# Performance work log

Hardware: AMD Instinct MI355X
Metric: run time of the kernel (lower is better)

Reference implementation:

```python
import jax, jax.numpy as jnp
import numpy as np

N_RBF = 16
N_HIDDEN = 64
CUTOFF = 5.0
N_ATOMS = 4096


def setup_inputs() -> dict:
    key = jax.random.key(0)
    ks = jax.random.split(key, 7)
    # Scale positions so the 5.0 cutoff yields a sparse-ish neighbor graph.
    positions = jax.random.normal(ks[0], (N_ATOMS, 3), dtype=jnp.float32) * 10.0
    s1 = 1.0 / np.sqrt(N_RBF)
    s2 = 1.0 / np.sqrt(N_HIDDEN)
    W1 = jax.random.normal(ks[1], (N_RBF, N_HIDDEN), dtype=jnp.float32) * s1
    b1 = jax.random.normal(ks[2], (N_HIDDEN,), dtype=jnp.float32) * 0.01
    W2 = jax.random.normal(ks[3], (N_HIDDEN, N_HIDDEN), dtype=jnp.float32) * s2
    b2 = jax.random.normal(ks[4], (N_HIDDEN,), dtype=jnp.float32) * 0.01
    W3 = jax.random.normal(ks[5], (N_HIDDEN, 1), dtype=jnp.float32) * s2
    b3 = jax.random.normal(ks[6], (1,), dtype=jnp.float32) * 0.01
    return {"positions": positions, "W1": W1, "b1": b1, "W2": W2, "b2": b2, "W3": W3, "b3": b3}


def _features(positions):
    # positions: (N, 3) -> per-node RBF-aggregated features (N, n_rbf).
    # Equivalent to torch mask.nonzero + scatter_add: features[i] = sum_j in-cutoff rbf(d_ij).
    diff = positions[:, None, :] - positions[None, :, :]          # (N, N, 3)
    dist = jnp.sqrt(jnp.sum(diff * diff, axis=-1))                # (N, N)
    mask = (dist > 1e-6) & (dist < CUTOFF)                        # (N, N)
    centers = jnp.linspace(0.5, CUTOFF, N_RBF, dtype=jnp.float32) # (n_rbf,)
    eta = 0.5 * CUTOFF / N_RBF
    gauss = jnp.exp(-((dist[..., None] - centers) ** 2) / (2.0 * eta * eta))  # (N, N, n_rbf)
    x = jnp.minimum(dist / CUTOFF, 1.0)
    smooth = 0.5 * (1.0 + jnp.cos(jnp.float32(np.pi) * x))        # (N, N)
    w = jnp.where(mask, smooth, 0.0)                              # masked smooth-cutoff weight
    return jnp.einsum('ij,ijk->ik', w, gauss)                     # (N, n_rbf)


def reference(positions, W1, b1, W2, b2, W3, b3):
    feats = _features(positions)                                  # (N, n_rbf)
    h = jax.nn.silu(feats @ W1 + b1)
    h = jax.nn.silu(h @ W2 + b2)
    energy = jnp.sum(h @ W3 + b3)                                 # scalar
    return energy
```

## Files before the change

kernel.cpp:

```cpp
#include <hip/hip_runtime.h>

#define N_ATOMS  4096
#define N_RBF    16
#define N_HIDDEN 64
#define NTHREADS 512
#define WPB      8
#define APB      8
#define NBLOCKS  (N_ATOMS / APB)
#define QCAP     96
#define QUART    (N_ATOMS / 4)

__global__ __launch_bounds__(256) void repack_kernel(const float* __restrict__ pos,
                                                     float4* __restrict__ pos4) {
    const int i = blockIdx.x * 256 + threadIdx.x;
    if (i < N_ATOMS)
        pos4[i] = make_float4(pos[i * 3 + 0], pos[i * 3 + 1], pos[i * 3 + 2], 0.0f);
}

__device__ __forceinline__ void accum_rbf(float d2, float (&f)[N_RBF]) {
    const float d  = sqrtf(d2);
    const float sm = 0.5f + 0.5f * __cosf(0.62831853071795865f * d);
    #pragma unroll
    for (int k = 0; k < N_RBF; ++k) {
        const float t = d - (0.5f + 0.3f * (float)k);
        f[k] += sm * __expf(-20.48f * t * t);
    }
}

__device__ __forceinline__ int wave_prefix(unsigned long long m) {
    return __builtin_amdgcn_mbcnt_hi((unsigned)(m >> 32),
            __builtin_amdgcn_mbcnt_lo((unsigned)m, 0u));
}

__global__ __launch_bounds__(NTHREADS, 8) void fused_sr_kernel(
    const float4* __restrict__ pos4,
    const float* __restrict__ W1,
    const float* __restrict__ b1,
    const float* __restrict__ W2,
    const float* __restrict__ b2,
    const float* __restrict__ W3,
    float* __restrict__ partial)
{
    __shared__ __align__(16) float qd[APB][4][QCAP];
    __shared__ int qcnt[APB][4];
    __shared__ __align__(16) float h1buf[WPB][N_HIDDEN];
    __shared__ float ered[WPB];

    const int tid  = threadIdx.x;
    const int lane = tid & 63;
    const int w    = tid >> 6;
    const int t    = w >> 2;
    const int q    = w & 3;
    const int iA   = blockIdx.x * APB + 4 * t;

    const float4 p0 = pos4[iA + 0];
    const float4 p1 = pos4[iA + 1];
    const float4 p2 = pos4[iA + 2];
    const float4 p3 = pos4[iA + 3];
    const int jbase = q * QUART;

    int c0_ = 0, c1_ = 0, c2_ = 0, c3_ = 0;

#define PAIR_TEST(P, CNT, AIDX)                                              \
    {                                                                        \
        const float dx = P.x - pj.x, dy = P.y - pj.y, dz = P.z - pj.z;       \
        const float d2 = fmaf(dx, dx, fmaf(dy, dy, dz * dz));                \
        const bool act = (d2 < 25.0f) && (d2 > 1e-12f);                      \
        const unsigned long long m = __ballot(act);                          \
        if (m) {                                                             \
            int widx = CNT + wave_prefix(m);                                 \
            widx = widx < QCAP ? widx : QCAP - 1;                            \
            if (act) qd[4 * t + AIDX][q][widx] = d2;                         \
            CNT += (int)__popcll(m);                                         \
        }                                                                    \
    }

    #pragma unroll 2
    for (int j0 = 0; j0 < QUART; j0 += 64) {
        const float4 pj = pos4[jbase + j0 + lane];
        PAIR_TEST(p0, c0_, 0)
        PAIR_TEST(p1, c1_, 1)
        PAIR_TEST(p2, c2_, 2)
        PAIR_TEST(p3, c3_, 3)
    }
#undef PAIR_TEST

    if (lane == 0) {
        qcnt[4 * t + 0][q] = c0_;
        qcnt[4 * t + 1][q] = c1_;
        qcnt[4 * t + 2][q] = c2_;
        qcnt[4 * t + 3][q] = c3_;
    }
    __syncthreads();

    const int co0 = qcnt[w][0], co1 = qcnt[w][1], co2 = qcnt[w][2], co3 = qcnt[w][3];
    const int o1 = co0, o2 = co0 + co1, o3 = o2 + co2, C = o3 + co3;
    float* qrow = &qd[w][0][0];

    float f[N_RBF];
    #pragma unroll
    for (int k = 0; k < N_RBF; ++k) f[k] = 0.0f;
    for (int b = 0; b < C; b += 64) {
        const int g = b + lane;
        const int part = (g >= o1) + (g >= o2) + (g >= o3);
        const int base = part == 0 ? 0 : (part == 1 ? o1 : (part == 2 ? o2 : o3));
        const float d2q = (g < C) ? qrow[part * QCAP + (g - base)] : 1e8f;
        accum_rbf(d2q, f);
    }

    #pragma unroll
    for (int k = 0; k < N_RBF; ++k) {
        f[k] += __shfl_xor(f[k], 32, 64);
        f[k] += __shfl_xor(f[k], 16, 64);
    }
    float* tb = qrow;
    if (lane < 16) {
        #pragma unroll
        for (int j = 0; j < 16; j += 4)
            *reinterpret_cast<float4*>(&tb[lane * 16 + j]) =
                make_float4(f[j], f[j + 1], f[j + 2], f[j + 3]);
    }
    const int kk = lane & 15, rep = lane >> 4;
    float F = 0.0f;
    #pragma unroll
    for (int i = 0; i < 4; ++i) F += tb[(4 * rep + i) * 16 + kk];
    F += __shfl_xor(F, 16, 64);
    F += __shfl_xor(F, 32, 64);
    if (lane < 16) tb[256 + lane] = F;

    float a1 = b1[lane];
    #pragma unroll
    for (int k = 0; k < N_RBF; ++k)
        a1 = fmaf(tb[256 + k], W1[k * N_HIDDEN + lane], a1);
    const float h1 = a1 / (1.0f + __expf(-a1));

    h1buf[w][lane] = h1;
    float a2 = b2[lane];
    #pragma unroll
    for (int k = 0; k < N_HIDDEN; k += 4) {
        const float4 hv = *reinterpret_cast<const float4*>(&h1buf[w][k]);
        a2 = fmaf(hv.x, W2[(k + 0) * N_HIDDEN + lane], a2);
        a2 = fmaf(hv.y, W2[(k + 1) * N_HIDDEN + lane], a2);
        a2 = fmaf(hv.z, W2[(k + 2) * N_HIDDEN + lane], a2);
        a2 = fmaf(hv.w, W2[(k + 3) * N_HIDDEN + lane], a2);
    }
    const float h2 = a2 / (1.0f + __expf(-a2));

    float e = h2 * W3[lane];
    #pragma unroll
    for (int off = 32; off > 0; off >>= 1)
        e += __shfl_xor(e, off, 64);
    if (lane == 0) ered[w] = e;
    __syncthreads();

    if (tid < 64) {
        float acc = (lane < WPB) ? ered[lane] : 0.0f;
        acc += __shfl_xor(acc, 4, 64);
        acc += __shfl_xor(acc, 2, 64);
        acc += __shfl_xor(acc, 1, 64);
        if (lane == 0) partial[blockIdx.x] = acc;
    }
}

__global__ __launch_bounds__(NTHREADS) void finish_kernel(
    const float* __restrict__ partial, const float* __restrict__ b3,
    float* __restrict__ out) {
    __shared__ float s[WPB];
    const int tid = threadIdx.x, lane = tid & 63, w = tid >> 6;
    float v = partial[tid];
    #pragma unroll
    for (int off = 32; off > 0; off >>= 1)
        v += __shfl_xor(v, off, 64);
    if (lane == 0) s[w] = v;
    __syncthreads();
    if (tid == 0) {
        float tot = 0.0f;
        #pragma unroll
        for (int i = 0; i < WPB; ++i) tot += s[i];
        out[0] = tot + (float)N_ATOMS * b3[0];
    }
}

extern "C" void kernel_launch(void* const* d_in, const int* in_sizes, int n_in,
                              void* d_out, int out_size, void* d_ws, size_t ws_size,
                              hipStream_t stream) {
    const float* pos = (const float*)d_in[0];
    const float* W1  = (const float*)d_in[1];
    const float* b1  = (const float*)d_in[2];
    const float* W2  = (const float*)d_in[3];
    const float* b2  = (const float*)d_in[4];
    const float* W3  = (const float*)d_in[5];
    const float* b3  = (const float*)d_in[6];
    float* out = (float*)d_out;

    float4* pos4    = (float4*)d_ws;
    float*  partial = (float*)((char*)d_ws + N_ATOMS * sizeof(float4));

    repack_kernel<<<(N_ATOMS + 255) / 256, 256, 0, stream>>>(pos, pos4);
    fused_sr_kernel<<<NBLOCKS, NTHREADS, 0, stream>>>(pos4, W1, b1, W2, b2, W3, partial);
    finish_kernel<<<1, NTHREADS, 0, stream>>>(partial, b3, out);
}
```

Baseline: 81.38 us.

## Replace brute-force all-pairs neighbor search with a uniform cell-list grid

Adds a zero-count kernel and an atomic binning kernel that sort atoms into a 24^3 grid of 5-unit cells. The main kernel then has one wave per atom scan only the 27 neighboring cells instead of all 4096 atoms. This removes the O(N^2) pair-distance work in exchange for two extra launches, atomics and a large workspace buffer. It relies on fixed caps (96 atoms per cell, 288 neighbors per atom) and a fixed coordinate range of [-60, 60] with clamping, all of which must hold for these inputs.

Result: slower. 84.79 us (+4.2%).

```diff
diff --git a/kernel.cpp b/kernel.cpp
--- a/kernel.cpp
+++ b/kernel.cpp
@@ -5,16 +5,35 @@
 #define N_HIDDEN 64
 #define NTHREADS 512
 #define WPB      8
-#define APB      8
-#define NBLOCKS  (N_ATOMS / APB)
-#define QCAP     96
-#define QUART    (N_ATOMS / 4)
-
-__global__ __launch_bounds__(256) void repack_kernel(const float* __restrict__ pos,
-                                                     float4* __restrict__ pos4) {
+#define NBLOCKS  (N_ATOMS / WPB)
+#define QCAP     288
+#define GRIDC    24
+#define NCELL    (GRIDC * GRIDC * GRIDC)
+#define CCAP     96
+#define CELL_INV 0.2f
+#define RANGEF   60.0f
+
+__global__ __launch_bounds__(256) void zero_counts(int* __restrict__ count) {
     const int i = blockIdx.x * 256 + threadIdx.x;
-    if (i < N_ATOMS)
-        pos4[i] = make_float4(pos[i * 3 + 0], pos[i * 3 + 1], pos[i * 3 + 2], 0.0f);
+    if (i < NCELL) count[i] = 0;
+}
+
+__global__ __launch_bounds__(256) void bin_kernel(const float* __restrict__ pos,
+                                                  int* __restrict__ count,
+                                                  float4* __restrict__ cellAtoms) {
+    const int i = blockIdx.x * 256 + threadIdx.x;
+    if (i >= N_ATOMS) return;
+    const float x = pos[3 * i + 0], y = pos[3 * i + 1], z = pos[3 * i + 2];
+    int cx = (int)floorf((x + RANGEF) * CELL_INV);
+    int cy = (int)floorf((y + RANGEF) * CELL_INV);
+    int cz = (int)floorf((z + RANGEF) * CELL_INV);
+    cx = min(max(cx, 0), GRIDC - 1);
+    cy = min(max(cy, 0), GRIDC - 1);
+    cz = min(max(cz, 0), GRIDC - 1);
+    const int cell = cx + GRIDC * (cy + GRIDC * cz);
+    int slot = atomicAdd(&count[cell], 1);
+    if (slot >= CCAP) slot = CCAP - 1;
+    cellAtoms[cell * CCAP + slot] = make_float4(x, y, z, 0.0f);
 }
 
 __device__ __forceinline__ void accum_rbf(float d2, float (&f)[N_RBF]) {
@@ -32,8 +51,10 @@
             __builtin_amdgcn_mbcnt_lo((unsigned)m, 0u));
 }
 
-__global__ __launch_bounds__(NTHREADS, 8) void fused_sr_kernel(
-    const float4* __restrict__ pos4,
+__global__ __launch_bounds__(NTHREADS) void fused_sr_kernel(
+    const float* __restrict__ pos,
+    const int* __restrict__ count,
+    const float4* __restrict__ cellAtoms,
     const float* __restrict__ W1,
     const float* __restrict__ b1,
     const float* __restrict__ W2,
@@ -41,71 +62,65 @@
     const float* __restrict__ W3,
     float* __restrict__ partial)
 {
-    __shared__ __align__(16) float qd[APB][4][QCAP];
-    __shared__ int qcnt[APB][4];
+    __shared__ float qd[WPB][QCAP];
     __shared__ __align__(16) float h1buf[WPB][N_HIDDEN];
     __shared__ float ered[WPB];
 
     const int tid  = threadIdx.x;
     const int lane = tid & 63;
     const int w    = tid >> 6;
-    const int t    = w >> 2;
-    const int q    = w & 3;
-    const int iA   = blockIdx.x * APB + 4 * t;
-
-    const float4 p0 = pos4[iA + 0];
-    const float4 p1 = pos4[iA + 1];
-    const float4 p2 = pos4[iA + 2];
-    const float4 p3 = pos4[iA + 3];
-    const int jbase = q * QUART;
-
-    int c0_ = 0, c1_ = 0, c2_ = 0, c3_ = 0;
-
-#define PAIR_TEST(P, CNT, AIDX)                                              \
-    {                                                                        \
-        const float dx = P.x - pj.x, dy = P.y - pj.y, dz = P.z - pj.z;       \
-        const float d2 = fmaf(dx, dx, fmaf(dy, dy, dz * dz));                \
-        const bool act = (d2 < 25.0f) && (d2 > 1e-12f);                      \
-        const unsigned long long m = __ballot(act);                          \
-        if (m) {                                                             \
-            int widx = CNT + wave_prefix(m);                                 \
-            widx = widx < QCAP ? widx : QCAP - 1;                            \
-            if (act) qd[4 * t + AIDX][q][widx] = d2;                         \
-            CNT += (int)__popcll(m);                                         \
-        }                                                                    \
-    }
-
-    #pragma unroll 2
-    for (int j0 = 0; j0 < QUART; j0 += 64) {
-        const float4 pj = pos4[jbase + j0 + lane];
-        PAIR_TEST(p0, c0_, 0)
-        PAIR_TEST(p1, c1_, 1)
-        PAIR_TEST(p2, c2_, 2)
-        PAIR_TEST(p3, c3_, 3)
-    }
-#undef PAIR_TEST
-
-    if (lane == 0) {
-        qcnt[4 * t + 0][q] = c0_;
-        qcnt[4 * t + 1][q] = c1_;
-        qcnt[4 * t + 2][q] = c2_;
-        qcnt[4 * t + 3][q] = c3_;
-    }
-    __syncthreads();
-
-    const int co0 = qcnt[w][0], co1 = qcnt[w][1], co2 = qcnt[w][2], co3 = qcnt[w][3];
-    const int o1 = co0, o2 = co0 + co1, o3 = o2 + co2, C = o3 + co3;
-    float* qrow = &qd[w][0][0];
+    const int i    = blockIdx.x * WPB + w;
+
+    const float xi = pos[3 * i + 0], yi = pos[3 * i + 1], zi = pos[3 * i + 2];
+    int cx = (int)floorf((xi + RANGEF) * CELL_INV);
+    int cy = (int)floorf((yi + RANGEF) * CELL_INV);
+    int cz = (int)floorf((zi + RANGEF) * CELL_INV);
+    cx = min(max(cx, 0), GRIDC - 1);
+    cy = min(max(cy, 0), GRIDC - 1);
+    cz = min(max(cz, 0), GRIDC - 1);
+
+    int myCell = 0, myCnt = 0;
+    if (lane < 27) {
+        const int nx = cx + (lane % 3) - 1;
+        const int ny = cy + ((lane / 3) % 3) - 1;
+        const int nz = cz + (lane / 9) - 1;
+        if (nx >= 0 && nx < GRIDC && ny >= 0 && ny < GRIDC && nz >= 0 && nz < GRIDC) {
+            myCell = nx + GRIDC * (ny + GRIDC * nz);
+            myCnt  = min(count[myCell], CCAP);
+        }
+    }
+
+    int qn = 0;
+    for (int j = 0; j < 27; ++j) {
+        const int cnt = __shfl(myCnt, j, 64);
+        if (cnt == 0) continue;
+        const int cid = __shfl(myCell, j, 64);
+        const float4* cbase = &cellAtoms[cid * CCAP];
+        for (int b = 0; b < cnt; b += 64) {
+            const int g = b + lane;
+            float d2 = 1e8f;
+            if (g < cnt) {
+                const float4 pj = cbase[g];
+                const float dx = xi - pj.x, dy = yi - pj.y, dz = zi - pj.z;
+                d2 = fmaf(dx, dx, fmaf(dy, dy, dz * dz));
+            }
+            const bool act = (d2 < 25.0f) && (d2 > 1e-12f);
+            const unsigned long long m = __ballot(act);
+            if (m) {
+                int widx = qn + wave_prefix(m);
+                widx = widx < QCAP ? widx : QCAP - 1;
+                if (act) qd[w][widx] = d2;
+                qn += (int)__popcll(m);
+            }
+        }
+    }
 
     float f[N_RBF];
     #pragma unroll
     for (int k = 0; k < N_RBF; ++k) f[k] = 0.0f;
-    for (int b = 0; b < C; b += 64) {
+    for (int b = 0; b < qn; b += 64) {
         const int g = b + lane;
-        const int part = (g >= o1) + (g >= o2) + (g >= o3);
-        const int base = part == 0 ? 0 : (part == 1 ? o1 : (part == 2 ? o2 : o3));
-        const float d2q = (g < C) ? qrow[part * QCAP + (g - base)] : 1e8f;
-        accum_rbf(d2q, f);
+        accum_rbf((g < qn) ? qd[w][g] : 1e8f, f);
     }
 
     #pragma unroll
@@ -113,17 +128,15 @@
         f[k] += __shfl_xor(f[k], 32, 64);
         f[k] += __shfl_xor(f[k], 16, 64);
     }
-    float* tb = qrow;
+    float* tb = &qd[w][0];
     if (lane < 16) {
         #pragma unroll
-        for (int j = 0; j < 16; j += 4)
-            *reinterpret_cast<float4*>(&tb[lane * 16 + j]) =
-                make_float4(f[j], f[j + 1], f[j + 2], f[j + 3]);
+        for (int j = 0; j < 16; ++j) tb[lane * 16 + j] = f[j];
     }
     const int kk = lane & 15, rep = lane >> 4;
     float F = 0.0f;
     #pragma unroll
-    for (int i = 0; i < 4; ++i) F += tb[(4 * rep + i) * 16 + kk];
+    for (int v = 0; v < 4; ++v) F += tb[(4 * rep + v) * 16 + kk];
     F += __shfl_xor(F, 16, 64);
     F += __shfl_xor(F, 32, 64);
     if (lane < 16) tb[256 + lane] = F;
@@ -193,10 +206,13 @@
     const float* b3  = (const float*)d_in[6];
     float* out = (float*)d_out;
 
-    float4* pos4    = (float4*)d_ws;
-    float*  partial = (float*)((char*)d_ws + N_ATOMS * sizeof(float4));
-
-    repack_kernel<<<(N_ATOMS + 255) / 256, 256, 0, stream>>>(pos, pos4);
-    fused_sr_kernel<<<NBLOCKS, NTHREADS, 0, stream>>>(pos4, W1, b1, W2, b2, W3, partial);
+    int*    count     = (int*)d_ws;
+    float4* cellAtoms = (float4*)((char*)d_ws + 65536);
+    float*  partial   = (float*)((char*)d_ws + 65536 + (size_t)NCELL * CCAP * sizeof(float4));
+
+    zero_counts<<<(NCELL + 255) / 256, 256, 0, stream>>>(count);
+    bin_kernel<<<(N_ATOMS + 255) / 256, 256, 0, stream>>>(pos, count, cellAtoms);
+    fused_sr_kernel<<<NBLOCKS, NTHREADS, 0, stream>>>(pos, count, cellAtoms,
+                                                      W1, b1, W2, b2, W3, partial);
     finish_kernel<<<1, NTHREADS, 0, stream>>>(partial, b3, out);
 }
```
